# Optimization experiments

Hardware: AMD Instinct MI355X
Metric: run time of the kernel (lower is better)

The kernel has to match this reference:

```python
import jax, jax.numpy as jnp
import numpy as np

DIM = 512
HEADS = 8
HEAD_DIM = DIM // HEADS
SR = 2
LN_EPS = 1e-3  # keras LayerNormalization default epsilon


def setup_inputs() -> dict:
    key = jax.random.key(0)
    ks = jax.random.split(key, 12)
    B, N = 4, 64 * 64
    s = lambda fan_in: 1.0 / np.sqrt(fan_in)
    return {
        "x": jax.random.normal(ks[0], (B, N, DIM), dtype=jnp.float32),
        "H": 64,
        "W": 64,
        "Wq": jax.random.normal(ks[1], (DIM, DIM), jnp.float32) * s(DIM),
        "bq": jnp.zeros((DIM,), jnp.float32),
        "Wkv": jax.random.normal(ks[2], (DIM, 2 * DIM), jnp.float32) * s(DIM),
        "bkv": jnp.zeros((2 * DIM,), jnp.float32),
        "Wp": jax.random.normal(ks[3], (DIM, DIM), jnp.float32) * s(DIM),
        "bp": jnp.zeros((DIM,), jnp.float32),
        "sr_kernel": jax.random.normal(ks[4], (SR, SR, DIM, DIM), jnp.float32) * s(SR * SR * DIM),
        "sr_bias": jnp.zeros((DIM,), jnp.float32),
        "gamma": jnp.ones((DIM,), jnp.float32),
        "beta": jnp.zeros((DIM,), jnp.float32),
    }


def _layer_norm(x, gamma, beta):
    mu = jnp.mean(x, axis=-1, keepdims=True)
    var = jnp.mean(jnp.square(x - mu), axis=-1, keepdims=True)
    return (x - mu) * jax.lax.rsqrt(var + LN_EPS) * gamma + beta


def reference(x, H, W, Wq, bq, Wkv, bkv, Wp, bp, sr_kernel, sr_bias, gamma, beta):
    B, N, C = x.shape
    scale = HEAD_DIM ** -0.5

    # q projection -> [B, heads, N, head_dim]
    q = (x @ Wq + bq).reshape(B, N, HEADS, HEAD_DIM).transpose(0, 2, 1, 3)

    # sequence reduction: strided conv (kernel=stride=SR, SAME padding) + LayerNorm
    x_ = x.reshape(B, H, W, C)
    x_ = jax.lax.conv_general_dilated(
        x_, sr_kernel, window_strides=(SR, SR), padding="SAME",
        dimension_numbers=("NHWC", "HWIO", "NHWC")) + sr_bias
    x_ = x_.reshape(B, -1, C)           # [B, N_kv, C]
    x_ = _layer_norm(x_, gamma, beta)

    # kv projection -> k, v: [B, heads, N_kv, head_dim]
    kv = (x_ @ Wkv + bkv).reshape(B, -1, 2, HEADS, HEAD_DIM).transpose(2, 0, 3, 1, 4)
    k, v = kv[0], kv[1]

    attn = jnp.einsum("bhnd,bhmd->bhnm", q, k) * scale
    attn = jax.nn.softmax(attn, axis=-1)
    out = jnp.einsum("bhnm,bhmd->bhnd", attn, v)  # [B, heads, N, head_dim]
    out = out.transpose(0, 2, 1, 3).reshape(B, N, C)
    return out @ Wp + bp
```

## Files before the change

kernel.cpp:

```cpp
#include <hip/hip_runtime.h>
#include <math.h>

#define BDIM   4
#define NTOK   4096
#define CDIM   512
#define NHEADS 8
#define HDIM   64
#define NKV    1024
#define HPIX   64
#define WPIX   64

typedef __attribute__((ext_vector_type(8)))  short    short8;
typedef __attribute__((ext_vector_type(4)))  float    floatx4;
typedef __attribute__((ext_vector_type(16))) float    floatx16;
typedef __attribute__((ext_vector_type(4)))  unsigned uintx4;
typedef unsigned short ushort_t;

static __device__ inline unsigned short f2bf(float f) {
  unsigned u = __float_as_uint(f);
  unsigned r = (u + 0x7fffu + ((u >> 16) & 1u)) >> 16;
  return (unsigned short)r;
}

static __device__ inline unsigned cvt_pk_bf16(float lo, float hi) {
  unsigned r;
  asm volatile("v_cvt_pk_bf16_f32 %0, %1, %2" : "=v"(r) : "v"(lo), "v"(hi));
  return r;
}

static __device__ inline void pl32_swap(unsigned& a, unsigned& b) {
  asm volatile("v_permlane32_swap_b32 %0, %1" : "+v"(a), "+v"(b));
}

static __device__ inline void gload16(const void* g, void* l) {
  __builtin_amdgcn_global_load_lds(
      (const __attribute__((address_space(1))) void*)g,
      (__attribute__((address_space(3))) void*)l, 16, 0, 0);
}

__global__ __launch_bounds__(256) void cvt_bf16(
    const float* __restrict__ in, ushort_t* __restrict__ out) {
  const size_t i = ((size_t)blockIdx.x * 256 + threadIdx.x) * 8;
  float4 f0 = *(const float4*)&in[i];
  float4 f1 = *(const float4*)&in[i + 4];
  short8 v;
  v[0] = (short)f2bf(f0.x); v[1] = (short)f2bf(f0.y);
  v[2] = (short)f2bf(f0.z); v[3] = (short)f2bf(f0.w);
  v[4] = (short)f2bf(f1.x); v[5] = (short)f2bf(f1.y);
  v[6] = (short)f2bf(f1.z); v[7] = (short)f2bf(f1.w);
  *(short8*)&out[i] = v;
}

__global__ __launch_bounds__(256) void transpose_cvt_all(
    const float* __restrict__ Wq, const float* __restrict__ Wkv,
    const float* __restrict__ Wp, const float* __restrict__ srk,
    ushort_t* __restrict__ Wqt, ushort_t* __restrict__ Wkvt,
    ushort_t* __restrict__ Wpt, ushort_t* __restrict__ srkt) {
  __shared__ float t[32][33];
  const int bid = blockIdx.x;
  const float* in; ushort_t* outp; int C, tile;
  if (bid < 256)       { in = Wq;  outp = Wqt;  C = 512;  tile = bid; }
  else if (bid < 768)  { in = Wkv; outp = Wkvt; C = 1024; tile = bid - 256; }
  else if (bid < 1024) { in = Wp;  outp = Wpt;  C = 512;  tile = bid - 768; }
  else                 { in = srk; outp = srkt; C = 512;  tile = bid - 1024; }
  const int R = (bid >= 1024) ? 2048 : 512;
  const int tcn = C >> 5;
  const int r0 = (tile / tcn) * 32, c0 = (tile % tcn) * 32;
  const int tr = threadIdx.x & 31, tc = threadIdx.x >> 5;
#pragma unroll
  for (int i = 0; i < 4; ++i)
    t[tc + 8 * i][tr] = in[(size_t)(r0 + tc + 8 * i) * C + c0 + tr];
  __syncthreads();
#pragma unroll
  for (int i = 0; i < 4; ++i)
    outp[(size_t)(c0 + tc + 8 * i) * R + r0 + tr] = f2bf(t[tr][tc + 8 * i]);
}

__global__ __launch_bounds__(256) void gemm_bf16(
    const ushort_t* __restrict__ A, const ushort_t* __restrict__ Bt,
    const float* __restrict__ bias, float* __restrict__ Cf,
    ushort_t* __restrict__ Cb, int M, int N, int K, float scale) {
  __shared__ char As[16384];
  __shared__ char Bs[16384];
  const int tid = threadIdx.x;
  const int w = tid >> 6, lane = tid & 63;
  const int g = lane >> 4, qr = lane & 15;
  const int wr = w >> 1, wc = w & 1;
  const int row0 = blockIdx.x * 128, col0 = blockIdx.y * 128;
  const int rl = w * 8 + (lane >> 3);
  const int sch = (lane & 7) ^ ((lane >> 3) & 7);

  floatx4 acc[4][4] = {};

  for (int k0 = 0; k0 < K; k0 += 64) {
    __syncthreads();
#pragma unroll
    for (int i = 0; i < 4; ++i) {
      const int r = rl + 32 * i;
      const unsigned lb = (unsigned)(w * 1024 + i * 4096);
      gload16(&A[(size_t)(row0 + r) * K + k0 + sch * 8], As + lb);
      gload16(&Bt[(size_t)(col0 + r) * K + k0 + sch * 8], Bs + lb);
    }
    __syncthreads();

#pragma unroll
    for (int kc = 0; kc < 2; ++kc) {
      short8 af[4], bfr[4];
#pragma unroll
      for (int mi = 0; mi < 4; ++mi) {
        const int r = wr * 64 + mi * 16 + qr;
        af[mi] = *(const short8*)(As +
            ((unsigned)(r * 128 + kc * 64 + g * 16) ^ (unsigned)((r & 7) << 4)));
      }
#pragma unroll
      for (int ni = 0; ni < 4; ++ni) {
        const int c = wc * 64 + ni * 16 + qr;
        bfr[ni] = *(const short8*)(Bs +
            ((unsigned)(c * 128 + kc * 64 + g * 16) ^ (unsigned)((c & 7) << 4)));
      }
#pragma unroll
      for (int mi = 0; mi < 4; ++mi)
#pragma unroll
        for (int ni = 0; ni < 4; ++ni)
          acc[mi][ni] = __builtin_amdgcn_mfma_f32_16x16x32_bf16(
              af[mi], bfr[ni], acc[mi][ni], 0, 0, 0);
    }
  }

#pragma unroll
  for (int mi = 0; mi < 4; ++mi) {
#pragma unroll
    for (int ni = 0; ni < 4; ++ni) {
      const int col = col0 + wc * 64 + ni * 16 + qr;
      const float bv = bias[col];
#pragma unroll
      for (int ri = 0; ri < 4; ++ri) {
        const int row = row0 + wr * 64 + mi * 16 + g * 4 + ri;
        const float v = (acc[mi][ni][ri] + bv) * scale;
        if (Cb) Cb[(size_t)row * N + col] = f2bf(v);
        else    Cf[(size_t)row * N + col] = v;
      }
    }
  }
}

__global__ __launch_bounds__(256) void gemm_kv(
    const ushort_t* __restrict__ A, const ushort_t* __restrict__ Bt,
    const float* __restrict__ bias, char* __restrict__ Kimg,
    char* __restrict__ Vimg) {
  __shared__ char As[16384];
  __shared__ char Bs[16384];
  const int tid = threadIdx.x;
  const int w = tid >> 6, lane = tid & 63;
  const int g = lane >> 4, qr = lane & 15;
  const int wr = w >> 1, wc = w & 1;
  const int row0 = blockIdx.x * 128, col0 = blockIdx.y * 128;
  const int rl = w * 8 + (lane >> 3);
  const int sch = (lane & 7) ^ ((lane >> 3) & 7);

  floatx4 acc[4][4] = {};

  for (int k0 = 0; k0 < 512; k0 += 64) {
    __syncthreads();
#pragma unroll
    for (int i = 0; i < 4; ++i) {
      const int r = rl + 32 * i;
      const unsigned lb = (unsigned)(w * 1024 + i * 4096);
      gload16(&A[(size_t)(row0 + r) * 512 + k0 + sch * 8], As + lb);
      gload16(&Bt[(size_t)(col0 + r) * 512 + k0 + sch * 8], Bs + lb);
    }
    __syncthreads();

#pragma unroll
    for (int kc = 0; kc < 2; ++kc) {
      short8 af[4], bfr[4];
#pragma unroll
      for (int mi = 0; mi < 4; ++mi) {
        const int r = wr * 64 + mi * 16 + qr;
        af[mi] = *(const short8*)(As +
            ((unsigned)(r * 128 + kc * 64 + g * 16) ^ (unsigned)((r & 7) << 4)));
      }
#pragma unroll
      for (int ni = 0; ni < 4; ++ni) {
        const int c = wc * 64 + ni * 16 + qr;
        bfr[ni] = *(const short8*)(Bs +
            ((unsigned)(c * 128 + kc * 64 + g * 16) ^ (unsigned)((c & 7) << 4)));
      }
#pragma unroll
      for (int mi = 0; mi < 4; ++mi)
#pragma unroll
        for (int ni = 0; ni < 4; ++ni)
          acc[mi][ni] = __builtin_amdgcn_mfma_f32_16x16x32_bf16(
              af[mi], bfr[ni], acc[mi][ni], 0, 0, 0);
    }
  }

#pragma unroll
  for (int mi = 0; mi < 4; ++mi) {
#pragma unroll
    for (int ni = 0; ni < 4; ++ni) {
      const int col = col0 + wc * 64 + ni * 16 + qr;
      const float bv = bias[col];
#pragma unroll
      for (int ri = 0; ri < 4; ++ri) {
        const int row = row0 + wr * 64 + mi * 16 + g * 4 + ri;
        const ushort_t v = f2bf(acc[mi][ni][ri] + bv);
        const int b = row >> 10, m = row & 1023;
        const int t = m >> 6, mr = m & 63;
        if (col < 512) {
          const int h = col >> 6, d = col & 63;
          char* img = Kimg + (((size_t)(b * NHEADS + h) * 16 + t) << 13);
          *(ushort_t*)(img + (unsigned)(mr * 128) +
                       ((unsigned)(2 * d) ^ (unsigned)((mr & 7) << 4))) = v;
        } else {
          const int c = col - 512, h = c >> 6, d = c & 63;
          char* img = Vimg + (((size_t)(b * NHEADS + h) * 16 + t) << 13);
          *(ushort_t*)(img + (unsigned)(d * 128) +
                       ((unsigned)(2 * mr) ^ (unsigned)((d & 7) << 4))) = v;
        }
      }
    }
  }
}

__global__ __launch_bounds__(256) void conv_gemm(
    const ushort_t* __restrict__ xb, const ushort_t* __restrict__ Bt,
    const float* __restrict__ bias, float* __restrict__ Cf) {
  __shared__ char As[16384];
  __shared__ char Bs[8192];
  const int tid = threadIdx.x;
  const int w = tid >> 6, lane = tid & 63;
  const int g = lane >> 4, qr = lane & 15;
  const int wr = w >> 1, wc = w & 1;
  const int row0 = blockIdx.x * 128, col0 = blockIdx.y * 64;
  const int rl = w * 8 + (lane >> 3);
  const int sch = (lane & 7) ^ ((lane >> 3) & 7);

  floatx4 acc[4][2] = {};

  for (int k0 = 0; k0 < 2048; k0 += 64) {
    __syncthreads();
    {
      const int di = k0 >> 10, dj = (k0 >> 9) & 1, cib = (k0 & 511) + sch * 8;
#pragma unroll
      for (int i = 0; i < 4; ++i) {
        const int r = rl + 32 * i;
        const int gr = row0 + r;
        const int bb = gr >> 10, p = gr & 1023;
        const int oi = p >> 5, oj = p & 31;
        const size_t off =
            ((size_t)((bb * HPIX + 2 * oi + di) * WPIX + 2 * oj + dj)) * CDIM + cib;
        gload16(&xb[off], As + (unsigned)(w * 1024 + i * 4096));
      }
#pragma unroll
      for (int i = 0; i < 2; ++i) {
        const int r = rl + 32 * i;
        gload16(&Bt[(size_t)(col0 + r) * 2048 + k0 + sch * 8],
                Bs + (unsigned)(w * 1024 + i * 4096));
      }
    }
    __syncthreads();

#pragma unroll
    for (int kc = 0; kc < 2; ++kc) {
      short8 af[4], bfr[2];
#pragma unroll
      for (int mi = 0; mi < 4; ++mi) {
        const int r = wr * 64 + mi * 16 + qr;
        af[mi] = *(const short8*)(As +
            ((unsigned)(r * 128 + kc * 64 + g * 16) ^ (unsigned)((r & 7) << 4)));
      }
#pragma unroll
      for (int ni = 0; ni < 2; ++ni) {
        const int c = wc * 32 + ni * 16 + qr;
        bfr[ni] = *(const short8*)(Bs +
            ((unsigned)(c * 128 + kc * 64 + g * 16) ^ (unsigned)((c & 7) << 4)));
      }
#pragma unroll
      for (int mi = 0; mi < 4; ++mi)
#pragma unroll
        for (int ni = 0; ni < 2; ++ni)
          acc[mi][ni] = __builtin_amdgcn_mfma_f32_16x16x32_bf16(
              af[mi], bfr[ni], acc[mi][ni], 0, 0, 0);
    }
  }

#pragma unroll
  for (int mi = 0; mi < 4; ++mi) {
#pragma unroll
    for (int ni = 0; ni < 2; ++ni) {
      const int col = col0 + wc * 32 + ni * 16 + qr;
      const float bv = bias[col];
#pragma unroll
      for (int ri = 0; ri < 4; ++ri) {
        const int row = row0 + wr * 64 + mi * 16 + g * 4 + ri;
        Cf[(size_t)row * 512 + col] = acc[mi][ni][ri] + bv;
      }
    }
  }
}

__global__ __launch_bounds__(256) void ln_kernel(
    const float* __restrict__ in, ushort_t* __restrict__ out,
    const float* __restrict__ gamma, const float* __restrict__ beta) {
  const int row = blockIdx.x * 4 + (threadIdx.x >> 6);
  const int lane = threadIdx.x & 63;
  const float* p = in + (size_t)row * CDIM;
  float v[8];
  float s = 0.f;
#pragma unroll
  for (int j = 0; j < 8; ++j) { v[j] = p[lane + j * 64]; s += v[j]; }
#pragma unroll
  for (int o = 32; o > 0; o >>= 1) s += __shfl_xor(s, o);
  const float mu = s * (1.0f / 512.0f);
  float vs = 0.f;
#pragma unroll
  for (int j = 0; j < 8; ++j) { const float d = v[j] - mu; vs += d * d; }
#pragma unroll
  for (int o = 32; o > 0; o >>= 1) vs += __shfl_xor(vs, o);
  const float rstd = rsqrtf(vs * (1.0f / 512.0f) + 1e-3f);
  ushort_t* q = out + (size_t)row * CDIM;
#pragma unroll
  for (int j = 0; j < 8; ++j) {
    const int c = lane + j * 64;
    q[c] = f2bf((v[j] - mu) * rstd * gamma[c] + beta[c]);
  }
}

__global__ __launch_bounds__(256) void attn_kernel(
    const ushort_t* __restrict__ Q, const char* __restrict__ Kimg,
    const char* __restrict__ Vimg, ushort_t* __restrict__ AO) {
  __shared__ char Ks[8192];
  __shared__ char Vt[8192];
  __shared__ float red[4][32];

  const int b = blockIdx.z, h = blockIdx.y;
  const int q0 = blockIdx.x * 128;
  const int tid = threadIdx.x;
  const int w = tid >> 6, lane = tid & 63;
  const int ql = lane & 31;
  const int hi = lane >> 5;
  const unsigned swz = (unsigned)((ql & 7) << 4);
  const unsigned woff = (unsigned)(w * 2048);

  short8 qf[4];
  {
    const ushort_t* qp = &Q[((size_t)(b * NTOK + q0 + 32 * w + ql)) * CDIM + h * HDIM];
#pragma unroll
    for (int ks = 0; ks < 4; ++ks)
      qf[ks] = *(const short8*)&qp[ks * 16 + hi * 8];
  }

  const char* kbase = Kimg + (((size_t)(b * NHEADS + h)) << 17);
  const char* vbase = Vimg + (((size_t)(b * NHEADS + h)) << 17);
  const unsigned lo16 = woff + (unsigned)(lane * 16);

  floatx16 Oacc[2] = {};
  float l0 = 0.f, l1 = 0.f;

  for (int t = 0; t < NKV / 64; ++t) {
    __syncthreads();
    {
      const char* kg = kbase + ((size_t)t << 13) + lo16;
      const char* vg = vbase + ((size_t)t << 13) + lo16;
      gload16(kg,        Ks + woff);
      gload16(kg + 1024, Ks + woff + 1024);
      gload16(vg,        Vt + woff);
      gload16(vg + 1024, Vt + woff + 1024);
    }
    __syncthreads();

    floatx16 sacc[2];
    __builtin_amdgcn_s_setprio(1);
#pragma unroll
    for (int st = 0; st < 2; ++st) {
      floatx16 s_ = {};
#pragma unroll
      for (int ks = 0; ks < 4; ++ks) {
        const int m = st * 32 + ql;
        short8 kf = *(const short8*)(Ks + (unsigned)(m * 128) +
                                     ((unsigned)(ks * 32 + hi * 16) ^ swz));
        s_ = __builtin_amdgcn_mfma_f32_32x32x16_bf16(kf, qf[ks], s_, 0, 0, 0);
      }
      sacc[st] = s_;
    }
    __builtin_amdgcn_s_setprio(0);

#pragma unroll
    for (int st = 0; st < 2; ++st) {
      unsigned W[8];
#pragma unroll
      for (int i = 0; i < 8; ++i) {
        const float pa = __builtin_amdgcn_exp2f(sacc[st][2 * i]);
        const float pb = __builtin_amdgcn_exp2f(sacc[st][2 * i + 1]);
        l0 += pa; l1 += pb;
        W[i] = cvt_pk_bf16(pa, pb);
      }
      pl32_swap(W[0], W[2]); pl32_swap(W[1], W[3]);
      pl32_swap(W[4], W[6]); pl32_swap(W[5], W[7]);
      uintx4 u0 = {W[0], W[1], W[2], W[3]};
      uintx4 u1 = {W[4], W[5], W[6], W[7]};
      const short8 pa0 = __builtin_bit_cast(short8, u0);
      const short8 pa1 = __builtin_bit_cast(short8, u1);
      __builtin_amdgcn_s_setprio(1);
#pragma unroll
      for (int db = 0; db < 2; ++db) {
        const int d = db * 32 + ql;
        const unsigned rowb = (unsigned)(d * 128);
        short8 v0 = *(const short8*)(Vt + rowb +
                                     ((unsigned)(st * 64 + hi * 16) ^ swz));
        short8 v1 = *(const short8*)(Vt + rowb +
                                     ((unsigned)(st * 64 + 32 + hi * 16) ^ swz));
        Oacc[db] = __builtin_amdgcn_mfma_f32_32x32x16_bf16(pa0, v0, Oacc[db], 0, 0, 0);
        Oacc[db] = __builtin_amdgcn_mfma_f32_32x32x16_bf16(pa1, v1, Oacc[db], 0, 0, 0);
      }
      __builtin_amdgcn_s_setprio(0);
    }
  }

  float lrun = l0 + l1;
  lrun += __shfl_xor(lrun, 32);
  if (hi == 0) red[w][ql] = 1.0f / lrun;
  asm volatile("s_waitcnt lgkmcnt(0)" ::: "memory");
  __builtin_amdgcn_sched_barrier(0);
#pragma unroll
  for (int r = 0; r < 16; ++r) {
    const int qrow = (r & 3) + 8 * (r >> 2) + 4 * hi;
    const float iv = red[w][qrow];
    const size_t rowoff =
        ((size_t)(b * NTOK + q0 + 32 * w + qrow)) * CDIM + h * HDIM;
    AO[rowoff + ql]      = f2bf(Oacc[0][r] * iv);
    AO[rowoff + 32 + ql] = f2bf(Oacc[1][r] * iv);
  }
}

extern "C" void kernel_launch(void* const* d_in, const int* in_sizes, int n_in,
                              void* d_out, int out_size, void* d_ws, size_t ws_size,
                              hipStream_t stream) {
  const float* x     = (const float*)d_in[0];
  const float* Wq    = (const float*)d_in[3];
  const float* bq    = (const float*)d_in[4];
  const float* Wkv   = (const float*)d_in[5];
  const float* bkv   = (const float*)d_in[6];
  const float* Wp    = (const float*)d_in[7];
  const float* bp    = (const float*)d_in[8];
  const float* srk   = (const float*)d_in[9];
  const float* srb   = (const float*)d_in[10];
  const float* gamma = (const float*)d_in[11];
  const float* beta  = (const float*)d_in[12];
  float* out = (float*)d_out;

  ushort_t* xb   = (ushort_t*)d_ws;
  ushort_t* Qb   = xb + (size_t)16384 * 512;
  ushort_t* AOb  = Qb + (size_t)16384 * 512;
  float*    XR   = (float*)(AOb + (size_t)16384 * 512);
  ushort_t* XL   = (ushort_t*)(XR + (size_t)4096 * 512);
  char*     Kimg = (char*)(XL + (size_t)4096 * 512);
  char*     Vimg = Kimg + (size_t)4 * 8 * 16 * 8192;
  ushort_t* Wqt  = (ushort_t*)(Vimg + (size_t)4 * 8 * 16 * 8192);
  ushort_t* Wkvt = Wqt + (size_t)512 * 512;
  ushort_t* Wpt  = Wkvt + (size_t)1024 * 512;
  ushort_t* srkt = Wpt + (size_t)512 * 512;

  cvt_bf16<<<(16384 * 512) / (256 * 8), 256, 0, stream>>>(x, xb);
  transpose_cvt_all<<<2048, 256, 0, stream>>>(
      Wq, Wkv, Wp, srk, Wqt, Wkvt, Wpt, srkt);

  gemm_bf16<<<dim3(16384 / 128, 512 / 128), 256, 0, stream>>>(
      xb, Wqt, bq, nullptr, Qb, 16384, 512, 512, 0.125f * 1.44269504f);
  conv_gemm<<<dim3(4096 / 128, 512 / 64), 256, 0, stream>>>(xb, srkt, srb, XR);
  ln_kernel<<<4096 / 4, 256, 0, stream>>>(XR, XL, gamma, beta);
  gemm_kv<<<dim3(4096 / 128, 1024 / 128), 256, 0, stream>>>(
      XL, Wkvt, bkv, Kimg, Vimg);
  attn_kernel<<<dim3(NTOK / 128, NHEADS, BDIM), 256, 0, stream>>>(Qb, Kimg, Vimg, AOb);
  gemm_bf16<<<dim3(16384 / 128, 512 / 128), 256, 0, stream>>>(
      AOb, Wpt, bp, out, nullptr, 16384, 512, 512, 1.0f);
}
```

Measured before the change: 145.1 us.

## Pre-fragment K/V images for direct lane loads and double KV tile per barrier

The KV projection epilogue now writes K and V in a layout that already matches the MFMA fragments, so each lane in the attention kernel reads a contiguous 16-byte chunk with no XOR swizzle arithmetic. The attention loop loads 128 KV rows per iteration into doubled LDS buffers, which halves the number of barrier/load phases. The x conversion and weight transpose kernels are merged into one launch. The price is twice the LDS per block, which may lower occupancy, and scattered 2-byte stores in the KV epilogue.

```diff
diff --git a/kernel.cpp b/kernel.cpp
--- a/kernel.cpp
+++ b/kernel.cpp
@@ -38,32 +38,33 @@
       (__attribute__((address_space(3))) void*)l, 16, 0, 0);
 }
 
-__global__ __launch_bounds__(256) void cvt_bf16(
-    const float* __restrict__ in, ushort_t* __restrict__ out) {
-  const size_t i = ((size_t)blockIdx.x * 256 + threadIdx.x) * 8;
-  float4 f0 = *(const float4*)&in[i];
-  float4 f1 = *(const float4*)&in[i + 4];
-  short8 v;
-  v[0] = (short)f2bf(f0.x); v[1] = (short)f2bf(f0.y);
-  v[2] = (short)f2bf(f0.z); v[3] = (short)f2bf(f0.w);
-  v[4] = (short)f2bf(f1.x); v[5] = (short)f2bf(f1.y);
-  v[6] = (short)f2bf(f1.z); v[7] = (short)f2bf(f1.w);
-  *(short8*)&out[i] = v;
-}
-
-__global__ __launch_bounds__(256) void transpose_cvt_all(
+__global__ __launch_bounds__(256) void prep_kernel(
+    const float* __restrict__ x, ushort_t* __restrict__ xb,
     const float* __restrict__ Wq, const float* __restrict__ Wkv,
     const float* __restrict__ Wp, const float* __restrict__ srk,
     ushort_t* __restrict__ Wqt, ushort_t* __restrict__ Wkvt,
     ushort_t* __restrict__ Wpt, ushort_t* __restrict__ srkt) {
+  const int bid = blockIdx.x;
+  if (bid < 4096) {
+    const size_t i = ((size_t)bid * 256 + threadIdx.x) * 8;
+    float4 f0 = *(const float4*)&x[i];
+    float4 f1 = *(const float4*)&x[i + 4];
+    short8 v;
+    v[0] = (short)f2bf(f0.x); v[1] = (short)f2bf(f0.y);
+    v[2] = (short)f2bf(f0.z); v[3] = (short)f2bf(f0.w);
+    v[4] = (short)f2bf(f1.x); v[5] = (short)f2bf(f1.y);
+    v[6] = (short)f2bf(f1.z); v[7] = (short)f2bf(f1.w);
+    *(short8*)&xb[i] = v;
+    return;
+  }
   __shared__ float t[32][33];
-  const int bid = blockIdx.x;
+  const int tb = bid - 4096;
   const float* in; ushort_t* outp; int C, tile;
-  if (bid < 256)       { in = Wq;  outp = Wqt;  C = 512;  tile = bid; }
-  else if (bid < 768)  { in = Wkv; outp = Wkvt; C = 1024; tile = bid - 256; }
-  else if (bid < 1024) { in = Wp;  outp = Wpt;  C = 512;  tile = bid - 768; }
-  else                 { in = srk; outp = srkt; C = 512;  tile = bid - 1024; }
-  const int R = (bid >= 1024) ? 2048 : 512;
+  if (tb < 256)       { in = Wq;  outp = Wqt;  C = 512;  tile = tb; }
+  else if (tb < 768)  { in = Wkv; outp = Wkvt; C = 1024; tile = tb - 256; }
+  else if (tb < 1024) { in = Wp;  outp = Wpt;  C = 512;  tile = tb - 768; }
+  else                { in = srk; outp = srkt; C = 512;  tile = tb - 1024; }
+  const int R = (tb >= 1024) ? 2048 : 512;
   const int tcn = C >> 5;
   const int r0 = (tile / tcn) * 32, c0 = (tile % tcn) * 32;
   const int tr = threadIdx.x & 31, tc = threadIdx.x >> 5;
@@ -207,16 +208,23 @@
         const ushort_t v = f2bf(acc[mi][ni][ri] + bv);
         const int b = row >> 10, m = row & 1023;
         const int t = m >> 6, mr = m & 63;
+        const int st = mr >> 5;
         if (col < 512) {
           const int h = col >> 6, d = col & 63;
+          const int ql = mr & 31;
+          const int ks = d >> 4, hi2 = (d >> 3) & 1, j = d & 7;
           char* img = Kimg + (((size_t)(b * NHEADS + h) * 16 + t) << 13);
-          *(ushort_t*)(img + (unsigned)(mr * 128) +
-                       ((unsigned)(2 * d) ^ (unsigned)((mr & 7) << 4))) = v;
+          *(ushort_t*)(img + (unsigned)(((st * 4 + ks) << 10) +
+                       ((hi2 << 5) + ql) * 16 + j * 2)) = v;
         } else {
           const int c = col - 512, h = c >> 6, d = c & 63;
+          const int r5 = mr & 31;
+          const int hf16 = r5 >> 4, rem = r5 & 15;
+          const int hi2 = rem >> 3, cc = (rem >> 1) & 3, odd = rem & 1;
+          const int db = d >> 5, ql = d & 31;
           char* img = Vimg + (((size_t)(b * NHEADS + h) * 16 + t) << 13);
-          *(ushort_t*)(img + (unsigned)(d * 128) +
-                       ((unsigned)(2 * mr) ^ (unsigned)((d & 7) << 4))) = v;
+          *(ushort_t*)(img + (unsigned)(((st * 4 + db * 2 + hf16) << 10) +
+                       ((hi2 << 5) + ql) * 16 + cc * 4 + odd * 2)) = v;
         }
       }
     }
@@ -330,8 +338,8 @@
 __global__ __launch_bounds__(256) void attn_kernel(
     const ushort_t* __restrict__ Q, const char* __restrict__ Kimg,
     const char* __restrict__ Vimg, ushort_t* __restrict__ AO) {
-  __shared__ char Ks[8192];
-  __shared__ char Vt[8192];
+  __shared__ char Ks[16384];
+  __shared__ char Vt[16384];
   __shared__ float red[4][32];
 
   const int b = blockIdx.z, h = blockIdx.y;
@@ -340,8 +348,7 @@
   const int w = tid >> 6, lane = tid & 63;
   const int ql = lane & 31;
   const int hi = lane >> 5;
-  const unsigned swz = (unsigned)((ql & 7) << 4);
-  const unsigned woff = (unsigned)(w * 2048);
+  const unsigned lbyte = (unsigned)(lane * 16);
 
   short8 qf[4];
   {
@@ -353,68 +360,70 @@
 
   const char* kbase = Kimg + (((size_t)(b * NHEADS + h)) << 17);
   const char* vbase = Vimg + (((size_t)(b * NHEADS + h)) << 17);
-  const unsigned lo16 = woff + (unsigned)(lane * 16);
 
   floatx16 Oacc[2] = {};
   float l0 = 0.f, l1 = 0.f;
 
-  for (int t = 0; t < NKV / 64; ++t) {
+  for (int t2 = 0; t2 < NKV / 128; ++t2) {
     __syncthreads();
     {
-      const char* kg = kbase + ((size_t)t << 13) + lo16;
-      const char* vg = vbase + ((size_t)t << 13) + lo16;
-      gload16(kg,        Ks + woff);
-      gload16(kg + 1024, Ks + woff + 1024);
-      gload16(vg,        Vt + woff);
-      gload16(vg + 1024, Vt + woff + 1024);
-    }
-    __syncthreads();
-
-    floatx16 sacc[2];
-    __builtin_amdgcn_s_setprio(1);
-#pragma unroll
-    for (int st = 0; st < 2; ++st) {
-      floatx16 s_ = {};
-#pragma unroll
-      for (int ks = 0; ks < 4; ++ks) {
-        const int m = st * 32 + ql;
-        short8 kf = *(const short8*)(Ks + (unsigned)(m * 128) +
-                                     ((unsigned)(ks * 32 + hi * 16) ^ swz));
-        s_ = __builtin_amdgcn_mfma_f32_32x32x16_bf16(kf, qf[ks], s_, 0, 0, 0);
-      }
-      sacc[st] = s_;
-    }
-    __builtin_amdgcn_s_setprio(0);
-
-#pragma unroll
-    for (int st = 0; st < 2; ++st) {
-      unsigned W[8];
-#pragma unroll
-      for (int i = 0; i < 8; ++i) {
-        const float pa = __builtin_amdgcn_exp2f(sacc[st][2 * i]);
-        const float pb = __builtin_amdgcn_exp2f(sacc[st][2 * i + 1]);
-        l0 += pa; l1 += pb;
-        W[i] = cvt_pk_bf16(pa, pb);
-      }
-      pl32_swap(W[0], W[2]); pl32_swap(W[1], W[3]);
-      pl32_swap(W[4], W[6]); pl32_swap(W[5], W[7]);
-      uintx4 u0 = {W[0], W[1], W[2], W[3]};
-      uintx4 u1 = {W[4], W[5], W[6], W[7]};
-      const short8 pa0 = __builtin_bit_cast(short8, u0);
-      const short8 pa1 = __builtin_bit_cast(short8, u1);
+      const char* kg = kbase + ((size_t)t2 << 14) + w * 4096 + lane * 16;
+      const char* vg = vbase + ((size_t)t2 << 14) + w * 4096 + lane * 16;
+      char* kd = Ks + w * 4096;
+      char* vd = Vt + w * 4096;
+#pragma unroll
+      for (int i = 0; i < 4; ++i) {
+        gload16(kg + i * 1024, kd + i * 1024);
+        gload16(vg + i * 1024, vd + i * 1024);
+      }
+    }
+    __syncthreads();
+
+#pragma unroll
+    for (int sub = 0; sub < 2; ++sub) {
+      const char* ksb = Ks + sub * 8192 + lbyte;
+      const char* vtb = Vt + sub * 8192 + lbyte;
+
+      floatx16 sacc[2];
       __builtin_amdgcn_s_setprio(1);
 #pragma unroll
-      for (int db = 0; db < 2; ++db) {
-        const int d = db * 32 + ql;
-        const unsigned rowb = (unsigned)(d * 128);
-        short8 v0 = *(const short8*)(Vt + rowb +
-                                     ((unsigned)(st * 64 + hi * 16) ^ swz));
-        short8 v1 = *(const short8*)(Vt + rowb +
-                                     ((unsigned)(st * 64 + 32 + hi * 16) ^ swz));
-        Oacc[db] = __builtin_amdgcn_mfma_f32_32x32x16_bf16(pa0, v0, Oacc[db], 0, 0, 0);
-        Oacc[db] = __builtin_amdgcn_mfma_f32_32x32x16_bf16(pa1, v1, Oacc[db], 0, 0, 0);
+      for (int st = 0; st < 2; ++st) {
+        floatx16 s_ = {};
+#pragma unroll
+        for (int ks = 0; ks < 4; ++ks) {
+          short8 kf = *(const short8*)(ksb + ((st * 4 + ks) << 10));
+          s_ = __builtin_amdgcn_mfma_f32_32x32x16_bf16(kf, qf[ks], s_, 0, 0, 0);
+        }
+        sacc[st] = s_;
       }
       __builtin_amdgcn_s_setprio(0);
+
+#pragma unroll
+      for (int st = 0; st < 2; ++st) {
+        unsigned W[8];
+#pragma unroll
+        for (int i = 0; i < 8; ++i) {
+          const float pa = __builtin_amdgcn_exp2f(sacc[st][2 * i]);
+          const float pb = __builtin_amdgcn_exp2f(sacc[st][2 * i + 1]);
+          l0 += pa; l1 += pb;
+          W[i] = cvt_pk_bf16(pa, pb);
+        }
+        pl32_swap(W[0], W[2]); pl32_swap(W[1], W[3]);
+        pl32_swap(W[4], W[6]); pl32_swap(W[5], W[7]);
+        uintx4 u0 = {W[0], W[1], W[2], W[3]};
+        uintx4 u1 = {W[4], W[5], W[6], W[7]};
+        const short8 pa0 = __builtin_bit_cast(short8, u0);
+        const short8 pa1 = __builtin_bit_cast(short8, u1);
+        __builtin_amdgcn_s_setprio(1);
+#pragma unroll
+        for (int db = 0; db < 2; ++db) {
+          short8 v0 = *(const short8*)(vtb + ((st * 4 + db * 2) << 10));
+          short8 v1 = *(const short8*)(vtb + ((st * 4 + db * 2 + 1) << 10));
+          Oacc[db] = __builtin_amdgcn_mfma_f32_32x32x16_bf16(pa0, v0, Oacc[db], 0, 0, 0);
+          Oacc[db] = __builtin_amdgcn_mfma_f32_32x32x16_bf16(pa1, v1, Oacc[db], 0, 0, 0);
+        }
+        __builtin_amdgcn_s_setprio(0);
+      }
     }
   }
 
@@ -462,9 +471,8 @@
   ushort_t* Wpt  = Wkvt + (size_t)1024 * 512;
   ushort_t* srkt = Wpt + (size_t)512 * 512;
 
-  cvt_bf16<<<(16384 * 512) / (256 * 8), 256, 0, stream>>>(x, xb);
-  transpose_cvt_all<<<2048, 256, 0, stream>>>(
-      Wq, Wkv, Wp, srk, Wqt, Wkvt, Wpt, srkt);
+  prep_kernel<<<4096 + 2048, 256, 0, stream>>>(
+      x, xb, Wq, Wkv, Wp, srk, Wqt, Wkvt, Wpt, srkt);
 
   gemm_bf16<<<dim3(16384 / 128, 512 / 128), 256, 0, stream>>>(
       xb, Wqt, bq, nullptr, Qb, 16384, 512, 512, 0.125f * 1.44269504f);
```

After: 139.3 us. 4.1% less time.
